# Optimization experiments

Hardware: AMD Instinct MI355X
Metric: run time of the kernel (lower is better)

The kernel has to match this reference:

```python
import jax, jax.numpy as jnp
import numpy as np

N, E, NS, NB = 25000, 400000, 4, 8
S0, V0 = 64, 32            # input: 64x0e + 32x1o
MS, MV = 96, 96            # message irreps: 96x0e + 96x1o
OS, OV = 128, 32           # post-linear_down/skip: (64+64)x0e + 32x1o
NIRR = S0 + V0             # node_feats.irreps.num_irreps = 96
AVG_NEIGH = 16.0
Y1 = float(np.sqrt(3.0 / (4.0 * np.pi)))  # integral-normalized l=1 SH coeff


def setup_inputs() -> dict:
    key = jax.random.key(0)
    k = jax.random.split(key, 15)
    return {
        'node_feats': jax.random.normal(k[0], (N, S0 + 3 * V0), jnp.float32),
        'vectors': jax.random.normal(k[1], (E, 3), jnp.float32),
        'rbf': jax.random.uniform(k[2], (E, NB), jnp.float32),
        'species': jax.random.randint(k[3], (N,), 0, NS, jnp.int32),
        'senders': jax.random.randint(k[4], (E,), 0, N, jnp.int32),
        'receivers': jax.random.randint(k[5], (E,), 0, N, jnp.int32),
        'W_up_s': jax.random.normal(k[6], (S0, S0), jnp.float32),
        'W_up_v': jax.random.normal(k[7], (V0, V0), jnp.float32),
        'W_mlp1': jax.random.normal(k[8], (NB, 64), jnp.float32),
        'W_mlp2': jax.random.normal(k[9], (64, 64), jnp.float32),
        'W_mlp3': jax.random.normal(k[10], (64, MS + MV), jnp.float32),
        'W_down_s': jax.random.normal(k[11], (MS, OS), jnp.float32),
        'W_down_v': jax.random.normal(k[12], (MV, OV), jnp.float32),
        'W_skip_s': jax.random.normal(k[13], (NS, S0, OS), jnp.float32),
        'W_skip_v': jax.random.normal(k[14], (NS, V0, OV), jnp.float32),
    }


def reference(node_feats, vectors, rbf, species, senders, receivers,
              W_up_s, W_up_v, W_mlp1, W_mlp2, W_mlp3,
              W_down_s, W_down_v, W_skip_s, W_skip_v):
    n = node_feats.shape[0]
    s = node_feats[:, :S0]                      # [N, 64]   0e
    v = node_feats[:, S0:].reshape(n, V0, 3)    # [N, 32,3] 1o

    # linear_up (per-irrep linear, 1/sqrt(fan_in) path normalization), then gather
    s_up = (s @ W_up_s) * (1.0 / jnp.sqrt(S0))
    v_up = jnp.einsum('nci,cd->ndi', v, W_up_v) * (1.0 / jnp.sqrt(V0))
    s_e = s_up[senders]                         # [E, 64]
    v_e = v_up[senders]                         # [E, 32, 3]

    # spherical harmonics l=1, normalize=True, 'integral' normalization
    y = Y1 * vectors / (jnp.linalg.norm(vectors, axis=-1, keepdims=True) + 1e-12)

    # tensor products filtered to output irreps + 0e
    tp_v = s_e[:, :, None] * y[:, None, :]                       # 0e x 1o -> 1o [E,64,3]
    tp_s = jnp.einsum('eci,ei->ec', v_e, y) * (1.0 / jnp.sqrt(3.0))  # 1o x 1o -> 0e [E,32]
    msg_s = jnp.concatenate([s_e, tp_s], axis=1)                 # [E, 96]
    msg_v = jnp.concatenate([v_e, tp_v], axis=1)                 # [E, 96, 3]

    # radial MLP -> per-edge, per-irrep mixing weights
    h = jax.nn.silu(rbf @ W_mlp1 * (1.0 / jnp.sqrt(NB)))
    h = jax.nn.silu(h @ W_mlp2 * (1.0 / 8.0))
    mix = h @ W_mlp3 * (1.0 / 8.0)                               # [E, 192]

    inv = 1.0 / NIRR
    msg_s = msg_s * mix[:, :MS] * inv
    msg_v = msg_v * (mix[:, MS:] * inv)[:, :, None]

    # scatter-sum to receivers, then normalize by sqrt(avg_num_neighbors)
    agg_s = jax.ops.segment_sum(msg_s, receivers, num_segments=n) / jnp.sqrt(AVG_NEIGH)
    agg_v = jax.ops.segment_sum(msg_v, receivers, num_segments=n) / jnp.sqrt(AVG_NEIGH)

    # linear_down to 128x0e + 32x1o
    out_s = agg_s @ W_down_s * (1.0 / jnp.sqrt(MS))
    out_v = jnp.einsum('nci,cd->ndi', agg_v, W_down_v) * (1.0 / jnp.sqrt(MV))

    # species-indexed skip connection (indexed linear)
    skip_s = jnp.einsum('nc,ncd->nd', s, W_skip_s[species]) * (1.0 / jnp.sqrt(S0))
    skip_v = jnp.einsum('nci,ncd->ndi', v, W_skip_v[species]) * (1.0 / jnp.sqrt(V0))

    f_s = out_s + skip_s                                         # [N, 128]
    f_v = out_v + skip_v                                         # [N, 32, 3]

    # equivariant gate: first 96 scalars activated, last 32 scalars gate the vectors
    act_s = jax.nn.silu(f_s[:, :OS - OV])
    gates = jax.nn.silu(f_s[:, OS - OV:])
    gated_v = f_v * gates[:, :, None]
    return jnp.concatenate([act_s, gated_v.reshape(n, OV * 3)], axis=1)  # [N, 192]
```

## Files before the change

kernel.cpp:

```cpp
#include <hip/hip_runtime.h>
#include <hip/hip_bf16.h>
#include <hip/hip_fp16.h>
#include <hip/hip_fp8.h>

#define NN 25000
#define EE 400000

#define SC_UP_S 0.125f
#define SC_UP_V 0.17677669529663689f
#define Y1C 0.48860251190291992f
#define SC_MLP1 0.35355339059327373f
#define SC_MLP2 0.125f
#define SC3 0.0013020833333333333f
#define INV_SQRT3 0.57735026918962584f
#define SC_DOWN 0.025515518153991442f
#define SC_SKIP_S 0.125f
#define SC_SKIP_V 0.17677669529663689f

typedef __attribute__((ext_vector_type(8))) short short8;
typedef __attribute__((ext_vector_type(4))) float f32x4;

#if defined(__has_builtin)
#if __has_builtin(__builtin_amdgcn_cvt_pk_fp8_f32)
#define HAS_HW_FP8_ENC 1
#endif
#if __has_builtin(__builtin_amdgcn_cvt_pk_f32_fp8)
#define HAS_HW_FP8_DEC 1
#endif
#endif
#ifndef HAS_HW_FP8_ENC
#define HAS_HW_FP8_ENC 0
#endif
#ifndef HAS_HW_FP8_DEC
#define HAS_HW_FP8_DEC 0
#endif

__device__ __forceinline__ float silu(float x) {
  return __fdividef(x, 1.f + __expf(-x));
}
__device__ __forceinline__ unsigned short f2bf(float f) {
  __hip_bfloat16 h = __float2bfloat16(f);
  return *reinterpret_cast<unsigned short*>(&h);
}
__device__ __forceinline__ float bf2f(unsigned short s) {
  return __uint_as_float(((unsigned)s) << 16);
}
__device__ __forceinline__ float bfe(short8 v, int idx) {
  return __uint_as_float(((unsigned)(unsigned short)v[idx]) << 16);
}
__device__ __forceinline__ unsigned packbf(float lo, float hi) {
  return ((unsigned)f2bf(hi) << 16) | (unsigned)f2bf(lo);
}
__device__ __forceinline__ unsigned char f2fp8_sw(float x) {
  __hip_fp8_e4m3 v(x);
  return (unsigned char)v.__x;
}
__device__ __forceinline__ unsigned f2fp8x2(float a, float b) {
#if HAS_HW_FP8_ENC
  return (unsigned)__builtin_amdgcn_cvt_pk_fp8_f32(a, b, 0, false);
#else
  return (unsigned)f2fp8_sw(a) | ((unsigned)f2fp8_sw(b) << 8);
#endif
}
__device__ __forceinline__ float fp82f_sw(unsigned b) {
  __hip_fp8_e4m3 t;
  t.__x = (__hip_fp8_storage_t)b;
  return (float)t;
}
__device__ __forceinline__ void fp8x4dec(unsigned w, float* o) {
#if HAS_HW_FP8_DEC
  auto lo = __builtin_amdgcn_cvt_pk_f32_fp8((int)w, false);
  auto hi = __builtin_amdgcn_cvt_pk_f32_fp8((int)w, true);
  o[0] = lo[0]; o[1] = lo[1]; o[2] = hi[0]; o[3] = hi[1];
#else
  o[0] = fp82f_sw(w & 0xFF);
  o[1] = fp82f_sw((w >> 8) & 0xFF);
  o[2] = fp82f_sw((w >> 16) & 0xFF);
  o[3] = fp82f_sw(w >> 24);
#endif
}

#define W_W1P 0
#define W_W2P 1024
#define W_W3B 3072
#define W_WDS 9216
#define W_WDV 15360
#define W_WSS 16896
#define W_WSV 33280
#define W_SUPB 35328
#define W_VUPB (W_SUPB + NN * 32)
#define W_DEG (W_VUPB + NN * 48)
#define W_PRE (W_DEG + NN)
#define W_CUR (W_PRE + NN + 8)
#define W_RNK (W_CUR + NN)
#define W_EDN (W_RNK + EE)
#define W_END (W_EDN + EE * 56)

__global__ __launch_bounds__(256) void transpose_weights(
    const float* __restrict__ W1, const float* __restrict__ W2,
    const float* __restrict__ W3, const float* __restrict__ Wds,
    const float* __restrict__ Wdv, const float* __restrict__ Wss,
    const float* __restrict__ Wsv, float* __restrict__ ws) {
  int t = blockIdx.x * 256 + threadIdx.x;
  int stride = gridDim.x * 256;
  unsigned short* W1p = (unsigned short*)(ws + W_W1P);
  unsigned short* W2p = (unsigned short*)(ws + W_W2P);
  unsigned short* W3b = (unsigned short*)(ws + W_W3B);
  unsigned short* Wdsb = (unsigned short*)(ws + W_WDS);
  unsigned short* Wdvb = (unsigned short*)(ws + W_WDV);
  unsigned short* Wssb = (unsigned short*)(ws + W_WSS);
  unsigned short* Wsvb = (unsigned short*)(ws + W_WSV);
  for (int i = t; i < 2048; i += stride) {
    int c = i >> 5, k = i & 31;
    W1p[i] = (k < 8) ? f2bf(W1[k * 64 + c] * SC_MLP1) : (unsigned short)0;
  }
  for (int i = t; i < 4096; i += stride) {
    int c = i >> 6, k = i & 63;
    W2p[i] = f2bf(W2[k * 64 + c] * SC_MLP2);
  }
  for (int i = t; i < 12288; i += stride) {
    int c = i >> 6, k = i & 63;
    float sc = (c >= 64 && c < 96) ? (SC3 * INV_SQRT3) : SC3;
    W3b[i] = f2bf(W3[k * 192 + c] * sc);
  }
  for (int i = t; i < 12288; i += stride) {
    int o = i / 96, k = i - 96 * o;
    Wdsb[i] = f2bf(Wds[k * 128 + o] * SC_DOWN);
  }
  for (int i = t; i < 3072; i += stride) {
    int o = i / 96, k = i - 96 * o;
    Wdvb[i] = f2bf(Wdv[k * 32 + o] * SC_DOWN);
  }
  for (int i = t; i < 32768; i += stride)
    Wssb[i] = f2bf(Wss[i] * SC_SKIP_S);
  for (int i = t; i < 4096; i += stride)
    Wsvb[i] = f2bf(Wsv[i] * SC_SKIP_V);
}

__global__ __launch_bounds__(256) void up_kernel(
    const float* __restrict__ nf, const float* __restrict__ Wus,
    const float* __restrict__ Wuv, unsigned short* __restrict__ s_upb,
    unsigned short* __restrict__ v_upb) {
  int n = blockIdx.x;
  int t = threadIdx.x;
  __shared__ float sv[160];
  if (t < 160) sv[t] = nf[n * 160 + t];
  __syncthreads();
  if (t < 64) {
    float a = 0.f;
#pragma unroll
    for (int k = 0; k < 64; k++) a += sv[k] * Wus[k * 64 + t];
    s_upb[n * 64 + t] = f2bf(a * SC_UP_S);
  } else if (t < 160) {
    int j = t - 64;
    int c = j / 3, i = j - 3 * c;
    float a = 0.f;
#pragma unroll
    for (int k = 0; k < 32; k++) a += sv[64 + k * 3 + i] * Wuv[k * 32 + c];
    v_upb[n * 96 + j] = f2bf(a * SC_UP_V);
  }
}

__global__ __launch_bounds__(256) void count_deg(
    const int* __restrict__ receivers, int* __restrict__ deg) {
  int e = blockIdx.x * 256 + threadIdx.x;
  if (e < EE) atomicAdd(&deg[receivers[e]], 1);
}

__global__ __launch_bounds__(1024) void scan_kernel(
    const int* __restrict__ deg, int* __restrict__ prefix,
    int* __restrict__ cursor) {
  __shared__ int waveSums[16];
  __shared__ int sCarry;
  int t = threadIdx.x;
  int lane = t & 63, wv = t >> 6;
  if (t == 0) sCarry = 0;
  __syncthreads();
  for (int base = 0; base < NN; base += 1024) {
    int i = base + t;
    int x = (i < NN) ? deg[i] : 0;
    int v = x;
#pragma unroll
    for (int d = 1; d < 64; d <<= 1) {
      int u = __shfl_up(v, d, 64);
      if (lane >= d) v += u;
    }
    if (lane == 63) waveSums[wv] = v;
    __syncthreads();
    if (wv == 0 && lane < 16) {
      int s = waveSums[lane];
#pragma unroll
      for (int d = 1; d < 16; d <<= 1) {
        int u = __shfl_up(s, d, 64);
        if (lane >= d) s += u;
      }
      waveSums[lane] = s;
    }
    __syncthreads();
    int waveOff = (wv == 0) ? 0 : waveSums[wv - 1];
    int incl = v + waveOff + sCarry;
    if (i < NN) {
      prefix[i] = incl - x;
      cursor[i] = incl - x;
    }
    __syncthreads();
    if (t == 1023) sCarry = incl;
    __syncthreads();
  }
  if (t == 0) prefix[NN] = sCarry;
}

__global__ __launch_bounds__(256) void rank_kernel(
    const int* __restrict__ receivers, int* __restrict__ cursor,
    int* __restrict__ rankArr) {
  int e = blockIdx.x * 256 + threadIdx.x;
  if (e < EE) {
    int r = receivers[e];
    rankArr[e] = atomicAdd(&cursor[r], 1);
  }
}

__global__ __launch_bounds__(256, 4) void edge_down4(
    const float* __restrict__ rbf, const float* __restrict__ vectors,
    const int* __restrict__ senders, const int* __restrict__ rankArr,
    const unsigned short* __restrict__ W1p,
    const unsigned short* __restrict__ W2p,
    const unsigned short* __restrict__ W3b,
    const unsigned short* __restrict__ Wdsb,
    const unsigned short* __restrict__ Wdvb,
    const unsigned short* __restrict__ s_upb,
    const unsigned short* __restrict__ v_upb,
    unsigned char* __restrict__ edown) {
  __shared__ unsigned short sH[64 * 72];
  __shared__ unsigned short sMix[64 * 200];
  __shared__ int sRank[64];

  int t = threadIdx.x;
  int pbase = blockIdx.x * 64;
  int lane = t & 63;
  int wv = t >> 6;
  int rl = lane & 15;
  int kgrp = lane >> 4;
  int arow = 16 * wv + rl;
  int crow = 16 * wv + kgrp * 4;

  union S8 { short8 v; unsigned u[4]; };

  if (t < 64) sRank[t] = rankArr[pbase + t];
  int eid = pbase + arow;
  int snd = senders[eid];
  const unsigned short* seb = s_upb + (size_t)snd * 64;
  const unsigned short* veb = v_upb + (size_t)snd * 96;
  short8 se0 = *(const short8*)&seb[kgrp * 8];
  short8 se1 = *(const short8*)&seb[32 + kgrp * 8];
  short8 ve0 = *(const short8*)&veb[24 * kgrp];
  short8 ve1 = *(const short8*)&veb[24 * kgrp + 8];
  short8 ve2 = *(const short8*)&veb[24 * kgrp + 16];
  float vx = vectors[(size_t)eid * 3 + 0];
  float vy = vectors[(size_t)eid * 3 + 1];
  float vz = vectors[(size_t)eid * 3 + 2];
  float nrm = sqrtf(vx * vx + vy * vy + vz * vz) + 1e-12f;
  float ysc = Y1C / nrm;
  float y0 = vx * ysc, y1 = vy * ysc, y2 = vz * ysc;

  S8 a1;
  a1.u[0] = a1.u[1] = a1.u[2] = a1.u[3] = 0u;
  if (kgrp == 0) {
    float4 ra = *(const float4*)(rbf + (size_t)eid * 8);
    float4 rb = *(const float4*)(rbf + (size_t)eid * 8 + 4);
    a1.u[0] = packbf(ra.x, ra.y);
    a1.u[1] = packbf(ra.z, ra.w);
    a1.u[2] = packbf(rb.x, rb.y);
    a1.u[3] = packbf(rb.z, rb.w);
  }
#pragma unroll
  for (int ct = 0; ct < 4; ct++) {
    short8 b = *(const short8*)&W1p[(ct * 16 + rl) * 32 + kgrp * 8];
    f32x4 acc = {0.f, 0.f, 0.f, 0.f};
    acc = __builtin_amdgcn_mfma_f32_16x16x32_bf16(a1.v, b, acc, 0, 0, 0);
#pragma unroll
    for (int rr = 0; rr < 4; rr++)
      sH[(crow + rr) * 72 + ct * 16 + rl] = f2bf(silu(acc[rr]));
  }

  {
    short8 a20 = *(const short8*)&sH[arow * 72 + kgrp * 8];
    short8 a21 = *(const short8*)&sH[arow * 72 + 32 + kgrp * 8];
    short8 b0s[4], b1s[4];
#pragma unroll
    for (int ct = 0; ct < 4; ct++) {
      const unsigned short* wb = &W2p[(ct * 16 + rl) * 64];
      b0s[ct] = *(const short8*)&wb[kgrp * 8];
      b1s[ct] = *(const short8*)&wb[32 + kgrp * 8];
    }
#pragma unroll
    for (int ct = 0; ct < 4; ct++) {
      f32x4 acc = {0.f, 0.f, 0.f, 0.f};
      acc = __builtin_amdgcn_mfma_f32_16x16x32_bf16(a20, b0s[ct], acc, 0, 0, 0);
      acc = __builtin_amdgcn_mfma_f32_16x16x32_bf16(a21, b1s[ct], acc, 0, 0, 0);
#pragma unroll
      for (int rr = 0; rr < 4; rr++)
        sH[(crow + rr) * 72 + ct * 16 + rl] = f2bf(silu(acc[rr]));
    }
  }

  {
    short8 a30 = *(const short8*)&sH[arow * 72 + kgrp * 8];
    short8 a31 = *(const short8*)&sH[arow * 72 + 32 + kgrp * 8];
#pragma unroll
    for (int half = 0; half < 2; half++) {
      short8 b0s[6], b1s[6];
#pragma unroll
      for (int j = 0; j < 6; j++) {
        int cc = (half * 6 + j) * 16 + rl;
        const unsigned short* wb = &W3b[cc * 64];
        b0s[j] = *(const short8*)&wb[kgrp * 8];
        b1s[j] = *(const short8*)&wb[32 + kgrp * 8];
      }
#pragma unroll
      for (int j = 0; j < 6; j++) {
        int cc = (half * 6 + j) * 16 + rl;
        f32x4 acc = {0.f, 0.f, 0.f, 0.f};
        acc = __builtin_amdgcn_mfma_f32_16x16x32_bf16(a30, b0s[j], acc, 0, 0, 0);
        acc = __builtin_amdgcn_mfma_f32_16x16x32_bf16(a31, b1s[j], acc, 0, 0, 0);
#pragma unroll
        for (int rr = 0; rr < 4; rr++)
          sMix[(crow + rr) * 200 + cc] = f2bf(acc[rr]);
      }
    }
  }

  const unsigned short* mrow = &sMix[arow * 200];
  S8 as0, as1, as2, mvp1, mvp2, mvp3;
  {
    short8 m = *(const short8*)&mrow[kgrp * 8];
#pragma unroll
    for (int q = 0; q < 4; q++)
      as0.u[q] = packbf(bfe(se0, 2 * q) * bfe(m, 2 * q),
                        bfe(se0, 2 * q + 1) * bfe(m, 2 * q + 1));
  }
  {
    short8 m = *(const short8*)&mrow[32 + kgrp * 8];
#pragma unroll
    for (int q = 0; q < 4; q++)
      as1.u[q] = packbf(bfe(se1, 2 * q) * bfe(m, 2 * q),
                        bfe(se1, 2 * q + 1) * bfe(m, 2 * q + 1));
  }
  {
    short8 m = *(const short8*)&mrow[64 + kgrp * 8];
#pragma unroll
    for (int q = 0; q < 4; q++) {
      float e0, e1, e2, f0, f1, f2;
      if (6 * q < 8) e0 = bfe(ve0, 6 * q); else if (6 * q < 16) e0 = bfe(ve1, 6 * q - 8); else e0 = bfe(ve2, 6 * q - 16);
      if (6 * q + 1 < 8) e1 = bfe(ve0, 6 * q + 1); else if (6 * q + 1 < 16) e1 = bfe(ve1, 6 * q - 7); else e1 = bfe(ve2, 6 * q - 15);
      if (6 * q + 2 < 8) e2 = bfe(ve0, 6 * q + 2); else if (6 * q + 2 < 16) e2 = bfe(ve1, 6 * q - 6); else e2 = bfe(ve2, 6 * q - 14);
      if (6 * q + 3 < 8) f0 = bfe(ve0, 6 * q + 3); else if (6 * q + 3 < 16) f0 = bfe(ve1, 6 * q - 5); else f0 = bfe(ve2, 6 * q - 13);
      if (6 * q + 4 < 8) f1 = bfe(ve0, 6 * q + 4); else if (6 * q + 4 < 16) f1 = bfe(ve1, 6 * q - 4); else f1 = bfe(ve2, 6 * q - 12);
      if (6 * q + 5 < 8) f2 = bfe(ve0, 6 * q + 5); else if (6 * q + 5 < 16) f2 = bfe(ve1, 6 * q - 3); else f2 = bfe(ve2, 6 * q - 11);
      float da = e0 * y0 + e1 * y1 + e2 * y2;
      float db = f0 * y0 + f1 * y1 + f2 * y2;
      as2.u[q] = packbf(da * bfe(m, 2 * q), db * bfe(m, 2 * q + 1));
    }
  }
  mvp1.v = *(const short8*)&mrow[96 + kgrp * 8];
  mvp2.v = *(const short8*)&mrow[128 + kgrp * 8];
  mvp3.v = *(const short8*)&mrow[160 + kgrp * 8];
  __syncthreads();

  unsigned char* edL = (unsigned char*)sMix;
#pragma unroll
  for (int half = 0; half < 2; half++) {
    short8 b0s[4], b1s[4], b2s[4];
#pragma unroll
    for (int j = 0; j < 4; j++) {
      int col = (half * 4 + j) * 16 + rl;
      const unsigned short* wb = &Wdsb[col * 96];
      b0s[j] = *(const short8*)&wb[kgrp * 8];
      b1s[j] = *(const short8*)&wb[32 + kgrp * 8];
      b2s[j] = *(const short8*)&wb[64 + kgrp * 8];
    }
#pragma unroll
    for (int j = 0; j < 4; j++) {
      int col = (half * 4 + j) * 16 + rl;
      f32x4 acc = {0.f, 0.f, 0.f, 0.f};
      acc = __builtin_amdgcn_mfma_f32_16x16x32_bf16(as0.v, b0s[j], acc, 0, 0, 0);
      acc = __builtin_amdgcn_mfma_f32_16x16x32_bf16(as1.v, b1s[j], acc, 0, 0, 0);
      acc = __builtin_amdgcn_mfma_f32_16x16x32_bf16(as2.v, b2s[j], acc, 0, 0, 0);
      unsigned p01 = f2fp8x2(acc[0], acc[1]);
      unsigned p23 = f2fp8x2(acc[2], acc[3]);
      edL[(crow + 0) * 232 + col] = (unsigned char)p01;
      edL[(crow + 1) * 232 + col] = (unsigned char)(p01 >> 8);
      edL[(crow + 2) * 232 + col] = (unsigned char)p23;
      edL[(crow + 3) * 232 + col] = (unsigned char)(p23 >> 8);
    }
  }
  float yarr[3] = {y0, y1, y2};
#pragma unroll
  for (int i = 0; i < 3; i++) {
    S8 av0, av1, av2;
#pragma unroll
    for (int q = 0; q < 4; q++) {
      float g0, g1;
      int ja = 6 * q + i, jb = 6 * q + 3 + i;
      if (ja < 8) g0 = bfe(ve0, ja); else if (ja < 16) g0 = bfe(ve1, ja - 8); else g0 = bfe(ve2, ja - 16);
      if (jb < 8) g1 = bfe(ve0, jb); else if (jb < 16) g1 = bfe(ve1, jb - 8); else g1 = bfe(ve2, jb - 16);
      av0.u[q] = packbf(g0 * bfe(mvp1.v, 2 * q), g1 * bfe(mvp1.v, 2 * q + 1));
      av1.u[q] = packbf(bfe(se0, 2 * q) * yarr[i] * bfe(mvp2.v, 2 * q),
                        bfe(se0, 2 * q + 1) * yarr[i] * bfe(mvp2.v, 2 * q + 1));
      av2.u[q] = packbf(bfe(se1, 2 * q) * yarr[i] * bfe(mvp3.v, 2 * q),
                        bfe(se1, 2 * q + 1) * yarr[i] * bfe(mvp3.v, 2 * q + 1));
    }
#pragma unroll
    for (int ot = 0; ot < 2; ot++) {
      int o = ot * 16 + rl;
      const unsigned short* wb = &Wdvb[o * 96];
      short8 b0 = *(const short8*)&wb[kgrp * 8];
      short8 b1 = *(const short8*)&wb[32 + kgrp * 8];
      short8 b2 = *(const short8*)&wb[64 + kgrp * 8];
      f32x4 acc = {0.f, 0.f, 0.f, 0.f};
      acc = __builtin_amdgcn_mfma_f32_16x16x32_bf16(av0.v, b0, acc, 0, 0, 0);
      acc = __builtin_amdgcn_mfma_f32_16x16x32_bf16(av1.v, b1, acc, 0, 0, 0);
      acc = __builtin_amdgcn_mfma_f32_16x16x32_bf16(av2.v, b2, acc, 0, 0, 0);
      unsigned p01 = f2fp8x2(acc[0], acc[1]);
      unsigned p23 = f2fp8x2(acc[2], acc[3]);
      edL[(crow + 0) * 232 + 128 + o * 3 + i] = (unsigned char)p01;
      edL[(crow + 1) * 232 + 128 + o * 3 + i] = (unsigned char)(p01 >> 8);
      edL[(crow + 2) * 232 + 128 + o * 3 + i] = (unsigned char)p23;
      edL[(crow + 3) * 232 + 128 + o * 3 + i] = (unsigned char)(p23 >> 8);
    }
  }
  __syncthreads();

  {
    int row = t >> 2, q = t & 3;
    const unsigned* src = (const unsigned*)(edL + row * 232 + q * 56);
    unsigned* dst = (unsigned*)(edown + (size_t)sRank[row] * 224 + q * 56);
#pragma unroll
    for (int j = 0; j < 14; j++) dst[j] = src[j];
  }
}

__global__ __launch_bounds__(256) void gather_out4(
    const float* __restrict__ nf, const int* __restrict__ species,
    const int* __restrict__ prefix, const unsigned char* __restrict__ edown,
    const unsigned short* __restrict__ Wssb,
    const unsigned short* __restrict__ Wsvb, float* __restrict__ out) {
  int n = blockIdx.x;
  int t = threadIdx.x;
  __shared__ float sNF[160];
  __shared__ float sPart[16 * 224];
  __shared__ float sEd[224];
  __shared__ float sF[224];
  if (t < 160) sNF[t] = nf[(size_t)n * 160 + t];
  int beg = prefix[n], end = prefix[n + 1];
  if (t < 224) {
    int u = t % 14, rg = t / 14;
    float a[16];
#pragma unroll
    for (int j = 0; j < 16; j++) a[j] = 0.f;
    for (int s = beg + rg; s < end; s += 16) {
      uint4 v = *(const uint4*)(edown + (size_t)s * 224 + u * 16);
      float d[4];
      fp8x4dec(v.x, d);
      a[0] += d[0]; a[1] += d[1]; a[2] += d[2]; a[3] += d[3];
      fp8x4dec(v.y, d);
      a[4] += d[0]; a[5] += d[1]; a[6] += d[2]; a[7] += d[3];
      fp8x4dec(v.z, d);
      a[8] += d[0]; a[9] += d[1]; a[10] += d[2]; a[11] += d[3];
      fp8x4dec(v.w, d);
      a[12] += d[0]; a[13] += d[1]; a[14] += d[2]; a[15] += d[3];
    }
#pragma unroll
    for (int j = 0; j < 16; j += 4)
      *(float4*)&sPart[rg * 224 + u * 16 + j] = *(float4*)&a[j];
  }
  __syncthreads();
  if (t < 224) {
    float s = 0.f;
#pragma unroll
    for (int rg = 0; rg < 16; rg++) s += sPart[rg * 224 + t];
    sEd[t] = s;
  }
  __syncthreads();
  int spec = species[n];
  if (t < 128) {
    const unsigned short* wsk = Wssb + (size_t)spec * 8192;
    float b = 0.f;
#pragma unroll
    for (int k = 0; k < 64; k++) b += sNF[k] * bf2f(wsk[k * 128 + t]);
    sF[t] = sEd[t] + b;
  } else if (t < 224) {
    int j = t - 128;
    int c = j / 3, i = j - 3 * c;
    const unsigned short* wsk = Wsvb + (size_t)spec * 1024;
    float b = 0.f;
#pragma unroll
    for (int k = 0; k < 32; k++) b += sNF[64 + k * 3 + i] * bf2f(wsk[k * 32 + c]);
    sF[t] = sEd[t] + b;
  }
  __syncthreads();
  if (t < 96) {
    out[(size_t)n * 192 + t] = silu(sF[t]);
  } else if (t < 192) {
    int j = t - 96;
    int c = j / 3;
    out[(size_t)n * 192 + t] = sF[128 + j] * silu(sF[96 + c]);
  }
}

extern "C" void kernel_launch(void* const* d_in, const int* in_sizes, int n_in,
                              void* d_out, int out_size, void* d_ws, size_t ws_size,
                              hipStream_t stream) {
  const float* nf = (const float*)d_in[0];
  const float* vectors = (const float*)d_in[1];
  const float* rbf = (const float*)d_in[2];
  const int* species = (const int*)d_in[3];
  const int* senders = (const int*)d_in[4];
  const int* receivers = (const int*)d_in[5];
  const float* Wus = (const float*)d_in[6];
  const float* Wuv = (const float*)d_in[7];
  const float* W1 = (const float*)d_in[8];
  const float* W2 = (const float*)d_in[9];
  const float* W3 = (const float*)d_in[10];
  const float* Wds = (const float*)d_in[11];
  const float* Wdv = (const float*)d_in[12];
  const float* Wss = (const float*)d_in[13];
  const float* Wsv = (const float*)d_in[14];

  float* ws = (float*)d_ws;
  const unsigned short* W1p = (const unsigned short*)(ws + W_W1P);
  const unsigned short* W2p = (const unsigned short*)(ws + W_W2P);
  const unsigned short* W3b = (const unsigned short*)(ws + W_W3B);
  const unsigned short* Wdsb = (const unsigned short*)(ws + W_WDS);
  const unsigned short* Wdvb = (const unsigned short*)(ws + W_WDV);
  const unsigned short* Wssb = (const unsigned short*)(ws + W_WSS);
  const unsigned short* Wsvb = (const unsigned short*)(ws + W_WSV);
  unsigned short* s_upb = (unsigned short*)(ws + W_SUPB);
  unsigned short* v_upb = (unsigned short*)(ws + W_VUPB);
  int* deg = (int*)(ws + W_DEG);
  int* prefix = (int*)(ws + W_PRE);
  int* cursor = (int*)(ws + W_CUR);
  int* rankArr = (int*)(ws + W_RNK);
  unsigned char* edown = (unsigned char*)(ws + W_EDN);
  float* out = (float*)d_out;

  transpose_weights<<<16, 256, 0, stream>>>(W1, W2, W3, Wds, Wdv, Wss, Wsv, ws);
  up_kernel<<<NN, 256, 0, stream>>>(nf, Wus, Wuv, s_upb, v_upb);

  hipMemsetAsync(deg, 0, (size_t)NN * sizeof(int), stream);
  count_deg<<<(EE + 255) / 256, 256, 0, stream>>>(receivers, deg);
  scan_kernel<<<1, 1024, 0, stream>>>(deg, prefix, cursor);
  rank_kernel<<<(EE + 255) / 256, 256, 0, stream>>>(receivers, cursor, rankArr);
  edge_down4<<<EE / 64, 256, 0, stream>>>(rbf, vectors, senders, rankArr, W1p,
                                          W2p, W3b, Wdsb, Wdvb, s_upb, v_upb,
                                          edown);
  gather_out4<<<NN, 256, 0, stream>>>(nf, species, prefix, edown, Wssb, Wsvb,
                                      out);
}
```

Baseline: 336.5 us.

## Store edge-down outputs directly from MFMA registers, alias LDS buffers, raise occupancy

The edge kernel swaps the MFMA operand order so each lane holds four consecutive output columns for one edge row. It then writes packed fp8 words straight to the rank-sorted global edge buffer, dropping the LDS staging tile, the extra barrier and the copy-out loop. The vector block is now laid out i-major instead of interleaved, and the gather kernel is adjusted to match. sH is aliased onto sMix and launch bounds are raised to 6 blocks per SM to cut LDS use and register budget. The cost is more scattered 4-byte global stores and possible register spills.

```diff
diff --git a/kernel.cpp b/kernel.cpp
--- a/kernel.cpp
+++ b/kernel.cpp
@@ -95,6 +95,7 @@
 #define W_RNK (W_CUR + NN)
 #define W_EDN (W_RNK + EE)
 #define W_END (W_EDN + EE * 56)
+
 
 __global__ __launch_bounds__(256) void transpose_weights(
     const float* __restrict__ W1, const float* __restrict__ W2,
@@ -220,7 +221,7 @@
   }
 }
 
-__global__ __launch_bounds__(256, 4) void edge_down4(
+__global__ __launch_bounds__(256, 6) void edge_down5(
     const float* __restrict__ rbf, const float* __restrict__ vectors,
     const int* __restrict__ senders, const int* __restrict__ rankArr,
     const unsigned short* __restrict__ W1p,
@@ -231,9 +232,8 @@
     const unsigned short* __restrict__ s_upb,
     const unsigned short* __restrict__ v_upb,
     unsigned char* __restrict__ edown) {
-  __shared__ unsigned short sH[64 * 72];
   __shared__ unsigned short sMix[64 * 200];
-  __shared__ int sRank[64];
+  unsigned short* sH = sMix;
 
   int t = threadIdx.x;
   int pbase = blockIdx.x * 64;
@@ -246,8 +246,8 @@
 
   union S8 { short8 v; unsigned u[4]; };
 
-  if (t < 64) sRank[t] = rankArr[pbase + t];
   int eid = pbase + arow;
+  int rk = rankArr[eid];
   int snd = senders[eid];
   const unsigned short* seb = s_upb + (size_t)snd * 64;
   const unsigned short* veb = v_upb + (size_t)snd * 96;
@@ -304,9 +304,10 @@
     }
   }
 
+  short8 a30 = *(const short8*)&sH[arow * 72 + kgrp * 8];
+  short8 a31 = *(const short8*)&sH[arow * 72 + 32 + kgrp * 8];
+  __syncthreads();
   {
-    short8 a30 = *(const short8*)&sH[arow * 72 + kgrp * 8];
-    short8 a31 = *(const short8*)&sH[arow * 72 + 32 + kgrp * 8];
 #pragma unroll
     for (int half = 0; half < 2; half++) {
       short8 b0s[6], b1s[6];
@@ -365,9 +366,8 @@
   mvp1.v = *(const short8*)&mrow[96 + kgrp * 8];
   mvp2.v = *(const short8*)&mrow[128 + kgrp * 8];
   mvp3.v = *(const short8*)&mrow[160 + kgrp * 8];
-  __syncthreads();
-
-  unsigned char* edL = (unsigned char*)sMix;
+
+  unsigned char* edR = edown + (size_t)rk * 224;
 #pragma unroll
   for (int half = 0; half < 2; half++) {
     short8 b0s[4], b1s[4], b2s[4];
@@ -381,17 +381,13 @@
     }
 #pragma unroll
     for (int j = 0; j < 4; j++) {
-      int col = (half * 4 + j) * 16 + rl;
       f32x4 acc = {0.f, 0.f, 0.f, 0.f};
-      acc = __builtin_amdgcn_mfma_f32_16x16x32_bf16(as0.v, b0s[j], acc, 0, 0, 0);
-      acc = __builtin_amdgcn_mfma_f32_16x16x32_bf16(as1.v, b1s[j], acc, 0, 0, 0);
-      acc = __builtin_amdgcn_mfma_f32_16x16x32_bf16(as2.v, b2s[j], acc, 0, 0, 0);
-      unsigned p01 = f2fp8x2(acc[0], acc[1]);
-      unsigned p23 = f2fp8x2(acc[2], acc[3]);
-      edL[(crow + 0) * 232 + col] = (unsigned char)p01;
-      edL[(crow + 1) * 232 + col] = (unsigned char)(p01 >> 8);
-      edL[(crow + 2) * 232 + col] = (unsigned char)p23;
-      edL[(crow + 3) * 232 + col] = (unsigned char)(p23 >> 8);
+      acc = __builtin_amdgcn_mfma_f32_16x16x32_bf16(b0s[j], as0.v, acc, 0, 0, 0);
+      acc = __builtin_amdgcn_mfma_f32_16x16x32_bf16(b1s[j], as1.v, acc, 0, 0, 0);
+      acc = __builtin_amdgcn_mfma_f32_16x16x32_bf16(b2s[j], as2.v, acc, 0, 0, 0);
+      unsigned d = (f2fp8x2(acc[0], acc[1]) & 0xFFFFu) |
+                   (f2fp8x2(acc[2], acc[3]) << 16);
+      *(unsigned*)(edR + (half * 4 + j) * 16 + kgrp * 4) = d;
     }
   }
   float yarr[3] = {y0, y1, y2};
@@ -418,29 +414,17 @@
       short8 b1 = *(const short8*)&wb[32 + kgrp * 8];
       short8 b2 = *(const short8*)&wb[64 + kgrp * 8];
       f32x4 acc = {0.f, 0.f, 0.f, 0.f};
-      acc = __builtin_amdgcn_mfma_f32_16x16x32_bf16(av0.v, b0, acc, 0, 0, 0);
-      acc = __builtin_amdgcn_mfma_f32_16x16x32_bf16(av1.v, b1, acc, 0, 0, 0);
-      acc = __builtin_amdgcn_mfma_f32_16x16x32_bf16(av2.v, b2, acc, 0, 0, 0);
-      unsigned p01 = f2fp8x2(acc[0], acc[1]);
-      unsigned p23 = f2fp8x2(acc[2], acc[3]);
-      edL[(crow + 0) * 232 + 128 + o * 3 + i] = (unsigned char)p01;
-      edL[(crow + 1) * 232 + 128 + o * 3 + i] = (unsigned char)(p01 >> 8);
-      edL[(crow + 2) * 232 + 128 + o * 3 + i] = (unsigned char)p23;
-      edL[(crow + 3) * 232 + 128 + o * 3 + i] = (unsigned char)(p23 >> 8);
-    }
-  }
-  __syncthreads();
-
-  {
-    int row = t >> 2, q = t & 3;
-    const unsigned* src = (const unsigned*)(edL + row * 232 + q * 56);
-    unsigned* dst = (unsigned*)(edown + (size_t)sRank[row] * 224 + q * 56);
-#pragma unroll
-    for (int j = 0; j < 14; j++) dst[j] = src[j];
-  }
-}
-
-__global__ __launch_bounds__(256) void gather_out4(
+      acc = __builtin_amdgcn_mfma_f32_16x16x32_bf16(b0, av0.v, acc, 0, 0, 0);
+      acc = __builtin_amdgcn_mfma_f32_16x16x32_bf16(b1, av1.v, acc, 0, 0, 0);
+      acc = __builtin_amdgcn_mfma_f32_16x16x32_bf16(b2, av2.v, acc, 0, 0, 0);
+      unsigned d = (f2fp8x2(acc[0], acc[1]) & 0xFFFFu) |
+                   (f2fp8x2(acc[2], acc[3]) << 16);
+      *(unsigned*)(edR + 128 + i * 32 + ot * 16 + kgrp * 4) = d;
+    }
+  }
+}
+
+__global__ __launch_bounds__(256) void gather_out5(
     const float* __restrict__ nf, const int* __restrict__ species,
     const int* __restrict__ prefix, const unsigned char* __restrict__ edown,
     const unsigned short* __restrict__ Wssb,
@@ -491,11 +475,11 @@
     sF[t] = sEd[t] + b;
   } else if (t < 224) {
     int j = t - 128;
-    int c = j / 3, i = j - 3 * c;
+    int i = j >> 5, o = j & 31;
     const unsigned short* wsk = Wsvb + (size_t)spec * 1024;
     float b = 0.f;
 #pragma unroll
-    for (int k = 0; k < 32; k++) b += sNF[64 + k * 3 + i] * bf2f(wsk[k * 32 + c]);
+    for (int k = 0; k < 32; k++) b += sNF[64 + k * 3 + i] * bf2f(wsk[k * 32 + o]);
     sF[t] = sEd[t] + b;
   }
   __syncthreads();
@@ -503,8 +487,9 @@
     out[(size_t)n * 192 + t] = silu(sF[t]);
   } else if (t < 192) {
     int j = t - 96;
-    int c = j / 3;
-    out[(size_t)n * 192 + t] = sF[128 + j] * silu(sF[96 + c]);
+    int o = j / 3, i = j - 3 * o;
+    float g = silu(sF[96 + o]);
+    out[(size_t)n * 192 + t] = sF[128 + i * 32 + o] * g;
   }
 }
 
@@ -551,9 +536,9 @@
   count_deg<<<(EE + 255) / 256, 256, 0, stream>>>(receivers, deg);
   scan_kernel<<<1, 1024, 0, stream>>>(deg, prefix, cursor);
   rank_kernel<<<(EE + 255) / 256, 256, 0, stream>>>(receivers, cursor, rankArr);
-  edge_down4<<<EE / 64, 256, 0, stream>>>(rbf, vectors, senders, rankArr, W1p,
+  edge_down5<<<EE / 64, 256, 0, stream>>>(rbf, vectors, senders, rankArr, W1p,
                                           W2p, W3b, Wdsb, Wdvb, s_upb, v_upb,
                                           edown);
-  gather_out4<<<NN, 256, 0, stream>>>(nf, species, prefix, edown, Wssb, Wsvb,
+  gather_out5<<<NN, 256, 0, stream>>>(nf, species, prefix, edown, Wssb, Wsvb,
                                       out);
 }
```

New measurement: 565.6 us. +68.1%, slower.
